# Kernel tuning notes

Measured on AMD Instinct MI355X. Metric: run time of the kernel, lower is better.

Reference implementation:

```python
import jax, jax.numpy as jnp
import numpy as np

B, D, H = 8192, 256, 64


def setup_inputs() -> dict:
    key = jax.random.key(0)
    ks = jax.random.split(key, 7)
    noise = jax.random.normal(ks[0], (B, D), dtype=jnp.float32)
    adj_logits = jax.random.normal(ks[1], (D, D), dtype=jnp.float32) * 0.1
    # stacked per-node mechanism params: Linear(D,H) -> SiLU -> Linear(H,1)
    W1 = jax.random.normal(ks[2], (D, H, D), dtype=jnp.float32) * (1.0 / np.sqrt(D))
    b1 = jax.random.normal(ks[3], (D, H), dtype=jnp.float32) * (1.0 / np.sqrt(D))
    W2 = jax.random.normal(ks[4], (D, H), dtype=jnp.float32) * (1.0 / np.sqrt(H))
    b2 = jax.random.normal(ks[5], (D,), dtype=jnp.float32) * (1.0 / np.sqrt(H))
    log_sigma = jnp.zeros((D,), dtype=jnp.float32)  # torch init: tensor(0.0)
    return {"noise": noise, "adj_logits": adj_logits, "W1": W1, "b1": b1,
            "W2": W2, "b2": b2, "log_sigma": log_sigma}


def reference(noise, adj_logits, W1, b1, W2, b2, log_sigma):
    d = adj_logits.shape[0]
    # differentiable adjacency: sigmoid(logits) with zeroed diagonal
    adj = jax.nn.sigmoid(adj_logits) * (1.0 - jnp.eye(d, dtype=adj_logits.dtype))
    bsz = noise.shape[0]
    z0 = jnp.zeros((bsz, d), dtype=noise.dtype)

    def step(z, xs):
        i, a_col, w1, bb1, w2, bb2, ls, n_i = xs
        pv = z * a_col[None, :]                       # [B, D] masked parent values
        h = jax.nn.silu(pv @ w1.T + bb1[None, :])     # [B, H]
        det = h @ w2 + bb2                            # [B]
        val = det + jnp.exp(ls) * n_i                 # [B]
        z = jax.lax.dynamic_update_slice(z, val[:, None], (0, i))
        return z, None

    xs = (jnp.arange(d), adj.T, W1, b1, W2, b2, log_sigma, noise.T)
    z, _ = jax.lax.scan(step, z0, xs)
    return z
```

## Files before the change

kernel.cpp:

```cpp
#include <hip/hip_runtime.h>
#include <math.h>

#define Dn 256
#define Hn 64

typedef __attribute__((ext_vector_type(8))) short short8;
typedef float floatx4 __attribute__((ext_vector_type(4)));

static __device__ __forceinline__ unsigned short f2bf(float x) {
    unsigned int u = __float_as_uint(x);
    unsigned int r = (u + 0x7fffu + ((u >> 16) & 1u)) >> 16;
    return (unsigned short)r;
}

__global__ __launch_bounds__(256) void prep_sgm(const float* __restrict__ adj,
                                                float* __restrict__ sgm) {
    const int i = blockIdx.x, j = threadIdx.x;
    float m = 0.f;
    if (j != i) m = 1.f / (1.f + __expf(-adj[(size_t)j * Dn + i]));
    sgm[(size_t)i * Dn + j] = m;
}

__global__ __launch_bounds__(256) void prep_wb(const float* __restrict__ W1,
                                               const float* __restrict__ sgm,
                                               unsigned short* __restrict__ Wb) {
    const int c = blockIdx.x, i = blockIdx.y;
    const int t = threadIdx.x;
    const int nb = t >> 6, l = t & 63;
    const int kk = nb * 16 + (l & 15);
    const int jb = c * 32 + ((l >> 4) & 3) * 8;
    const float* wp = W1 + ((size_t)i * Hn + kk) * Dn + jb;
    const float* sp = sgm + (size_t)i * Dn + jb;
    unsigned short v[8];
#pragma unroll
    for (int e = 0; e < 8; ++e) v[e] = f2bf(wp[e] * sp[e]);
    unsigned short* dst = Wb + ((((size_t)i * 8 + c) * 4 + nb) * 64 + l) * 8;
    *(short8*)dst = *(const short8*)v;
}

__global__ __launch_bounds__(256) void prep_nst(const float* __restrict__ noise,
                                                const float* __restrict__ ls,
                                                float* __restrict__ nsT, int B) {
    __shared__ float tile[64][65];
    const int bi = blockIdx.x * 64, dj = blockIdx.y * 64;
    const int t = threadIdx.x, c = t & 63, rq = t >> 6;
#pragma unroll
    for (int it = 0; it < 16; ++it) {
        int b = bi + it * 4 + rq;
        tile[it * 4 + rq][c] = noise[(size_t)b * Dn + dj + c];
    }
    __syncthreads();
#pragma unroll
    for (int it = 0; it < 16; ++it) {
        int d = dj + it * 4 + rq;
        float sg = __expf(ls[d]);
        nsT[(size_t)d * B + bi + c] = tile[c][it * 4 + rq] * sg;
    }
}

__global__ __launch_bounds__(128, 1) void scm_main(const unsigned short* __restrict__ Wb,
                                                   const float* __restrict__ b1,
                                                   const float* __restrict__ W2,
                                                   const float* __restrict__ b2,
                                                   const float* __restrict__ nsT,
                                                   float* __restrict__ out, int B) {
    __shared__ unsigned short zbf[32][264];
    const int t = threadIdx.x;
    const int w = t >> 6, l = t & 63;
    const int n = l & 15, q = l >> 4;
    const int rowbase = blockIdx.x * 32 + w * 16;

    for (int idx = l; idx < 16 * 132; idx += 64) {
        int r = idx / 132, cc = idx - r * 132;
        ((unsigned int*)zbf[w * 16 + r])[cc] = 0u;
    }

    const unsigned short* wb_l = Wb + (size_t)l * 8;
    const unsigned short* zrow_lds = &zbf[w * 16 + n][0];

    short8 af[8];
    short8 bf[8][4];
    float b1v[4], w2v[4], b2v;
    float4 nv;

    {
#pragma unroll
        for (int nb = 0; nb < 4; ++nb) bf[0][nb] = *(const short8*)(wb_l + nb * 512);
#pragma unroll
        for (int nb = 0; nb < 4; ++nb) {
            b1v[nb] = b1[nb * 16 + n];
            w2v[nb] = W2[nb * 16 + n];
        }
        nv  = *(const float4*)(nsT + rowbase + q * 4);
        b2v = b2[0];
    }

#pragma unroll
    for (int sec = 0; sec < 8; ++sec) {
        if (sec > 0) {
            af[sec - 1] = *(const short8*)(zrow_lds + (sec - 1) * 32 + q * 8);
            const unsigned short* wbp = wb_l + (size_t)(sec * 32) * 16384 + sec * 2048;
#pragma unroll
            for (int nb = 0; nb < 4; ++nb) bf[sec][nb] = *(const short8*)(wbp + nb * 512);
        }
#pragma unroll 1
        for (int ii = 0; ii < 32; ++ii) {
            const int i = sec * 32 + ii;

            short8 ain = *(const short8*)(zrow_lds + sec * 32 + q * 8);

            floatx4 zero4 = {0.f, 0.f, 0.f, 0.f};
            floatx4 acc[4];
#pragma unroll
            for (int nb = 0; nb < 4; ++nb) acc[nb] = zero4;

#pragma unroll
            for (int c = 0; c < 8; ++c)
                if (c < sec) {
#pragma unroll
                    for (int nb = 0; nb < 4; ++nb)
                        acc[nb] = __builtin_amdgcn_mfma_f32_16x16x32_bf16(af[c], bf[c][nb], acc[nb], 0, 0, 0);
                }
#pragma unroll
            for (int nb = 0; nb < 4; ++nb)
                acc[nb] = __builtin_amdgcn_mfma_f32_16x16x32_bf16(ain, bf[sec][nb], acc[nb], 0, 0, 0);

            float b1c[4], w2c[4], nvr[4];
            float b2c = b2v;
#pragma unroll
            for (int nb = 0; nb < 4; ++nb) { b1c[nb] = b1v[nb]; w2c[nb] = w2v[nb]; }
            nvr[0] = nv.x; nvr[1] = nv.y; nvr[2] = nv.z; nvr[3] = nv.w;

            {
                int ip = i + 1; if (ip > 255) ip = 255;
                const unsigned short* wbp = wb_l + (size_t)ip * 16384;
#pragma unroll
                for (int c = 0; c < 8; ++c)
                    if (c <= sec) {
#pragma unroll
                        for (int nb = 0; nb < 4; ++nb)
                            bf[c][nb] = *(const short8*)(wbp + c * 2048 + nb * 512);
                    }
#pragma unroll
                for (int nb = 0; nb < 4; ++nb) {
                    b1v[nb] = b1[ip * Hn + nb * 16 + n];
                    w2v[nb] = W2[ip * Hn + nb * 16 + n];
                }
                nv  = *(const float4*)(nsT + (size_t)ip * B + rowbase + q * 4);
                b2v = b2[ip];
            }

            float d[4];
#pragma unroll
            for (int r = 0; r < 4; ++r) {
                float s = 0.f;
#pragma unroll
                for (int nb = 0; nb < 4; ++nb) {
                    float h = acc[nb][r] + b1c[nb];
                    s += __fdividef(h, 1.f + __expf(-h)) * w2c[nb];
                }
                d[r] = s;
            }
#pragma unroll
            for (int m = 1; m <= 8; m <<= 1) {
#pragma unroll
                for (int r = 0; r < 4; ++r) d[r] += __shfl_xor(d[r], m);
            }
            float z[4];
#pragma unroll
            for (int r = 0; r < 4; ++r) z[r] = d[r] + b2c + nvr[r];

            int srcl = ((l & 15) >> 2) << 4;
            float t0 = __shfl(z[0], srcl), t1 = __shfl(z[1], srcl);
            float t2 = __shfl(z[2], srcl), t3 = __shfl(z[3], srcl);
            float za = (l & 1) ? t1 : t0;
            float zb = (l & 1) ? t3 : t2;
            float zrow = (l & 2) ? zb : za;

            if (q == 0) {
                zbf[w * 16 + n][i] = f2bf(zrow);
                out[(size_t)(rowbase + n) * Dn + i] = zrow;
            }
        }
    }
}

extern "C" void kernel_launch(void* const* d_in, const int* in_sizes, int n_in,
                              void* d_out, int out_size, void* d_ws, size_t ws_size,
                              hipStream_t stream) {
    const float* noise      = (const float*)d_in[0];
    const float* adj_logits = (const float*)d_in[1];
    const float* W1         = (const float*)d_in[2];
    const float* b1         = (const float*)d_in[3];
    const float* W2         = (const float*)d_in[4];
    const float* b2         = (const float*)d_in[5];
    const float* log_sigma  = (const float*)d_in[6];
    float* out = (float*)d_out;

    const int B = in_sizes[0] / Dn;
    unsigned short* Wb  = (unsigned short*)d_ws;
    float*          nsT = (float*)((char*)d_ws + (size_t)Dn * Dn * Hn * 2);
    float*          sgm = nsT;

    prep_sgm<<<dim3(Dn), 256, 0, stream>>>(adj_logits, sgm);
    prep_wb<<<dim3(8, Dn), 256, 0, stream>>>(W1, sgm, Wb);
    prep_nst<<<dim3(B / 64, Dn / 64), 256, 0, stream>>>(noise, log_sigma, nsT, B);
    scm_main<<<dim3(B / 32), 128, 0, stream>>>(Wb, b1, W2, b2, nsT, out, B);
}
```

Baseline: 382.0 us.

## Stage weights via async global-to-LDS DMA and keep z in registers

The main kernel stops loading per-node bf16 weight fragments straight into registers. Instead it double-buffers each node's weight block in shared memory using global_load_lds DMA, with a block barrier before every step. The z row is now packed into register fragments (ain/af) instead of an LDS buffer, output stores are grouped into float4 writes, and the accumulation is split into two accumulator chains for more MFMA parallelism. The sigmoid mask kernel is folded into prep_wb, which removes one launch. The cost is a __syncthreads on every one of the 256 sequential steps and higher shared-memory use.

```diff
diff --git a/kernel.cpp b/kernel.cpp
--- a/kernel.cpp
+++ b/kernel.cpp
@@ -13,16 +13,14 @@
     return (unsigned short)r;
 }
 
-__global__ __launch_bounds__(256) void prep_sgm(const float* __restrict__ adj,
-                                                float* __restrict__ sgm) {
-    const int i = blockIdx.x, j = threadIdx.x;
-    float m = 0.f;
-    if (j != i) m = 1.f / (1.f + __expf(-adj[(size_t)j * Dn + i]));
-    sgm[(size_t)i * Dn + j] = m;
+static __device__ __forceinline__ void dma16(const void* g, void* l) {
+    __builtin_amdgcn_global_load_lds(
+        (__attribute__((address_space(1))) void*)g,
+        (__attribute__((address_space(3))) void*)l, 16, 0, 0);
 }
 
 __global__ __launch_bounds__(256) void prep_wb(const float* __restrict__ W1,
-                                               const float* __restrict__ sgm,
+                                               const float* __restrict__ adj,
                                                unsigned short* __restrict__ Wb) {
     const int c = blockIdx.x, i = blockIdx.y;
     const int t = threadIdx.x;
@@ -30,10 +28,14 @@
     const int kk = nb * 16 + (l & 15);
     const int jb = c * 32 + ((l >> 4) & 3) * 8;
     const float* wp = W1 + ((size_t)i * Hn + kk) * Dn + jb;
-    const float* sp = sgm + (size_t)i * Dn + jb;
     unsigned short v[8];
 #pragma unroll
-    for (int e = 0; e < 8; ++e) v[e] = f2bf(wp[e] * sp[e]);
+    for (int e = 0; e < 8; ++e) {
+        int j = jb + e;
+        float m = 0.f;
+        if (j != i) m = 1.f / (1.f + __expf(-adj[(size_t)j * Dn + i]));
+        v[e] = f2bf(wp[e] * m);
+    }
     unsigned short* dst = Wb + ((((size_t)i * 8 + c) * 4 + nb) * 64 + l) * 8;
     *(short8*)dst = *(const short8*)v;
 }
@@ -64,122 +66,131 @@
                                                    const float* __restrict__ b2,
                                                    const float* __restrict__ nsT,
                                                    float* __restrict__ out, int B) {
-    __shared__ unsigned short zbf[32][264];
+    __shared__ unsigned char bbuf[2][32768];
     const int t = threadIdx.x;
     const int w = t >> 6, l = t & 63;
     const int n = l & 15, q = l >> 4;
     const int rowbase = blockIdx.x * 32 + w * 16;
-
-    for (int idx = l; idx < 16 * 132; idx += 64) {
-        int r = idx / 132, cc = idx - r * 132;
-        ((unsigned int*)zbf[w * 16 + r])[cc] = 0u;
-    }
-
-    const unsigned short* wb_l = Wb + (size_t)l * 8;
-    const unsigned short* zrow_lds = &zbf[w * 16 + n][0];
-
-    short8 af[8];
-    short8 bf[8][4];
-    float b1v[4], w2v[4], b2v;
-    float4 nv;
-
-    {
-#pragma unroll
-        for (int nb = 0; nb < 4; ++nb) bf[0][nb] = *(const short8*)(wb_l + nb * 512);
-#pragma unroll
-        for (int nb = 0; nb < 4; ++nb) {
-            b1v[nb] = b1[nb * 16 + n];
-            w2v[nb] = W2[nb * 16 + n];
-        }
-        nv  = *(const float4*)(nsT + rowbase + q * 4);
-        b2v = b2[0];
-    }
-
-#pragma unroll
+    const unsigned char* wbb = (const unsigned char*)Wb;
+
+    short8 af[7];
+    short8 ain = (short8)0;
+#pragma unroll
+    for (int c = 0; c < 7; ++c) af[c] = (short8)0;
+
+    float b1n[4], w2n[4], b2n;
+    float4 nvn;
+    float zout[4];
+
+    for (int f = w; f < 4; f += 2)
+        dma16(wbb + (size_t)f * 1024 + (size_t)l * 16, &bbuf[0][f * 1024]);
+#pragma unroll
+    for (int nb = 0; nb < 4; ++nb) {
+        b1n[nb] = b1[nb * 16 + n];
+        w2n[nb] = W2[nb * 16 + n];
+    }
+    nvn = *(const float4*)(nsT + rowbase + q * 4);
+    b2n = b2[0];
+
+#pragma unroll 1
     for (int sec = 0; sec < 8; ++sec) {
-        if (sec > 0) {
-            af[sec - 1] = *(const short8*)(zrow_lds + (sec - 1) * 32 + q * 8);
-            const unsigned short* wbp = wb_l + (size_t)(sec * 32) * 16384 + sec * 2048;
-#pragma unroll
-            for (int nb = 0; nb < 4; ++nb) bf[sec][nb] = *(const short8*)(wbp + nb * 512);
-        }
+#pragma unroll
+        for (int k2 = 0; k2 < 7; ++k2)
+            if (sec == k2 + 1) af[k2] = ain;
+        if (sec > 0) ain = (short8)0;
+
 #pragma unroll 1
-        for (int ii = 0; ii < 32; ++ii) {
-            const int i = sec * 32 + ii;
-
-            short8 ain = *(const short8*)(zrow_lds + sec * 32 + q * 8);
-
-            floatx4 zero4 = {0.f, 0.f, 0.f, 0.f};
-            floatx4 acc[4];
-#pragma unroll
-            for (int nb = 0; nb < 4; ++nb) acc[nb] = zero4;
-
-#pragma unroll
-            for (int c = 0; c < 8; ++c)
-                if (c < sec) {
-#pragma unroll
-                    for (int nb = 0; nb < 4; ++nb)
-                        acc[nb] = __builtin_amdgcn_mfma_f32_16x16x32_bf16(af[c], bf[c][nb], acc[nb], 0, 0, 0);
-                }
-#pragma unroll
-            for (int nb = 0; nb < 4; ++nb)
-                acc[nb] = __builtin_amdgcn_mfma_f32_16x16x32_bf16(ain, bf[sec][nb], acc[nb], 0, 0, 0);
-
-            float b1c[4], w2c[4], nvr[4];
-            float b2c = b2v;
-#pragma unroll
-            for (int nb = 0; nb < 4; ++nb) { b1c[nb] = b1v[nb]; w2c[nb] = w2v[nb]; }
-            nvr[0] = nv.x; nvr[1] = nv.y; nvr[2] = nv.z; nvr[3] = nv.w;
-
-            {
-                int ip = i + 1; if (ip > 255) ip = 255;
-                const unsigned short* wbp = wb_l + (size_t)ip * 16384;
-#pragma unroll
-                for (int c = 0; c < 8; ++c)
-                    if (c <= sec) {
-#pragma unroll
-                        for (int nb = 0; nb < 4; ++nb)
-                            bf[c][nb] = *(const short8*)(wbp + c * 2048 + nb * 512);
+        for (int o = 0; o < 4; ++o) {
+#pragma unroll
+            for (int e8 = 0; e8 < 8; ++e8) {
+                const int i = sec * 32 + o * 8 + e8;
+
+                __syncthreads();
+
+                {
+                    int ip = i + 1; if (ip > 255) ip = 255;
+                    int nf = ((ip >> 5) + 1) * 4;
+                    const unsigned char* src = wbb + (size_t)ip * 32768;
+                    unsigned char* dstb = &bbuf[(i + 1) & 1][0];
+                    for (int f = w; f < nf; f += 2)
+                        dma16(src + (size_t)f * 1024 + (size_t)l * 16, dstb + f * 1024);
+                }
+
+                float b1c[4], w2c[4], nvr[4];
+                float b2c = b2n;
+#pragma unroll
+                for (int nb = 0; nb < 4; ++nb) { b1c[nb] = b1n[nb]; w2c[nb] = w2n[nb]; }
+                nvr[0] = nvn.x; nvr[1] = nvn.y; nvr[2] = nvn.z; nvr[3] = nvn.w;
+                {
+                    int ip = i + 1; if (ip > 255) ip = 255;
+#pragma unroll
+                    for (int nb = 0; nb < 4; ++nb) {
+                        b1n[nb] = b1[ip * Hn + nb * 16 + n];
+                        w2n[nb] = W2[ip * Hn + nb * 16 + n];
+                    }
+                    nvn = *(const float4*)(nsT + (size_t)ip * B + rowbase + q * 4);
+                    b2n = b2[ip];
+                }
+
+                const unsigned char* lbase = &bbuf[i & 1][0];
+                floatx4 zero4 = {0.f, 0.f, 0.f, 0.f};
+                floatx4 accA[4], accB[4];
+#pragma unroll
+                for (int nb = 0; nb < 4; ++nb) { accA[nb] = zero4; accB[nb] = zero4; }
+
+#pragma unroll
+                for (int c = 0; c < 7; ++c)
+                    if (c < sec) {
+#pragma unroll
+                        for (int nb = 0; nb < 4; ++nb) {
+                            short8 bfr = *(const short8*)(lbase + (size_t)(c * 4 + nb) * 1024 + (size_t)l * 16);
+                            if (c & 1) accB[nb] = __builtin_amdgcn_mfma_f32_16x16x32_bf16(af[c], bfr, accB[nb], 0, 0, 0);
+                            else       accA[nb] = __builtin_amdgcn_mfma_f32_16x16x32_bf16(af[c], bfr, accA[nb], 0, 0, 0);
+                        }
                     }
 #pragma unroll
                 for (int nb = 0; nb < 4; ++nb) {
-                    b1v[nb] = b1[ip * Hn + nb * 16 + n];
-                    w2v[nb] = W2[ip * Hn + nb * 16 + n];
-                }
-                nv  = *(const float4*)(nsT + (size_t)ip * B + rowbase + q * 4);
-                b2v = b2[ip];
-            }
-
-            float d[4];
-#pragma unroll
-            for (int r = 0; r < 4; ++r) {
-                float s = 0.f;
-#pragma unroll
-                for (int nb = 0; nb < 4; ++nb) {
-                    float h = acc[nb][r] + b1c[nb];
-                    s += __fdividef(h, 1.f + __expf(-h)) * w2c[nb];
-                }
-                d[r] = s;
-            }
-#pragma unroll
-            for (int m = 1; m <= 8; m <<= 1) {
-#pragma unroll
-                for (int r = 0; r < 4; ++r) d[r] += __shfl_xor(d[r], m);
-            }
-            float z[4];
-#pragma unroll
-            for (int r = 0; r < 4; ++r) z[r] = d[r] + b2c + nvr[r];
-
-            int srcl = ((l & 15) >> 2) << 4;
-            float t0 = __shfl(z[0], srcl), t1 = __shfl(z[1], srcl);
-            float t2 = __shfl(z[2], srcl), t3 = __shfl(z[3], srcl);
-            float za = (l & 1) ? t1 : t0;
-            float zb = (l & 1) ? t3 : t2;
-            float zrow = (l & 2) ? zb : za;
-
-            if (q == 0) {
-                zbf[w * 16 + n][i] = f2bf(zrow);
-                out[(size_t)(rowbase + n) * Dn + i] = zrow;
+                    short8 bfr = *(const short8*)(lbase + (size_t)(sec * 4 + nb) * 1024 + (size_t)l * 16);
+                    accB[nb] = __builtin_amdgcn_mfma_f32_16x16x32_bf16(ain, bfr, accB[nb], 0, 0, 0);
+                }
+
+                float d[4];
+#pragma unroll
+                for (int r = 0; r < 4; ++r) {
+                    float s = 0.f;
+#pragma unroll
+                    for (int nb = 0; nb < 4; ++nb) {
+                        float h = accA[nb][r] + accB[nb][r] + b1c[nb];
+                        s += __fdividef(h, 1.f + __expf(-h)) * w2c[nb];
+                    }
+                    d[r] = s;
+                }
+#pragma unroll
+                for (int m = 1; m <= 8; m <<= 1) {
+#pragma unroll
+                    for (int r = 0; r < 4; ++r) d[r] += __shfl_xor(d[r], m);
+                }
+                float z[4];
+#pragma unroll
+                for (int r = 0; r < 4; ++r) z[r] = d[r] + b2c + nvr[r];
+
+                int srcl = ((l & 15) >> 2) << 4;
+                float t0 = __shfl(z[0], srcl), t1 = __shfl(z[1], srcl);
+                float t2 = __shfl(z[2], srcl), t3 = __shfl(z[3], srcl);
+                float za = (l & 1) ? t1 : t0;
+                float zb = (l & 1) ? t3 : t2;
+                float zrow = (l & 2) ? zb : za;
+
+                unsigned short zb16 = f2bf(zrow);
+                if (q == o) ain[e8] = (short)zb16;
+
+                zout[e8 & 3] = zrow;
+                if ((e8 & 3) == 3) {
+                    if (q == 0) {
+                        float4 v = make_float4(zout[0], zout[1], zout[2], zout[3]);
+                        *(float4*)(out + (size_t)(rowbase + n) * Dn + (i - 3)) = v;
+                    }
+                }
             }
         }
     }
@@ -200,10 +211,8 @@
     const int B = in_sizes[0] / Dn;
     unsigned short* Wb  = (unsigned short*)d_ws;
     float*          nsT = (float*)((char*)d_ws + (size_t)Dn * Dn * Hn * 2);
-    float*          sgm = nsT;
-
-    prep_sgm<<<dim3(Dn), 256, 0, stream>>>(adj_logits, sgm);
-    prep_wb<<<dim3(8, Dn), 256, 0, stream>>>(W1, sgm, Wb);
+
+    prep_wb<<<dim3(8, Dn), 256, 0, stream>>>(W1, adj_logits, Wb);
     prep_nst<<<dim3(B / 64, Dn / 64), 256, 0, stream>>>(noise, log_sigma, nsT, B);
     scm_main<<<dim3(B / 32), 128, 0, stream>>>(Wb, b1, W2, b2, nsT, out, B);
 }
```

New measurement: 592.7 us. 55.2% more time.
